# Optimization experiments

Hardware: AMD Instinct MI355X
Metric: run time of the kernel (lower is better)

## Reference

```python
import jax, jax.numpy as jnp
import numpy as np

HIDDEN = 512
NUM_HEADS = 8
HEAD_DIM = HIDDEN // NUM_HEADS


def setup_inputs() -> dict:
    key = jax.random.key(0)
    k1, k2 = jax.random.split(key)
    x = jax.random.normal(k1, (2, 2048, HIDDEN), dtype=jnp.float32)
    # torch Linear(h, 3h, bias=False): weight shape [3h, h], y = x @ W.T
    W_qkv = jax.random.normal(k2, (3 * HIDDEN, HIDDEN), dtype=jnp.float32) * (HIDDEN ** -0.5)
    return {"x": x, "W_qkv": W_qkv}


def reference(x, W_qkv):
    B, S, h = x.shape
    H, d = NUM_HEADS, HEAD_DIM
    temperature = (1.0 / d) ** 0.5  # sqrt(1/head_dim)
    qkv = x @ W_qkv.T  # [B, S, 3h]
    # Original chunks 3h into H pieces of size 3d (per-head interleaved QKV),
    # stacks on dim=1 -> [B, H, S, 3d], then splits into Q, K, V.
    qkv = qkv.reshape(B, S, H, 3 * d).transpose(0, 2, 1, 3)  # [B, H, S, 3d]
    q, k, v = jnp.split(qkv, 3, axis=-1)  # each [B, H, S, d]
    scores = jnp.einsum("bhqd,bhkd->bhqk", q * temperature, k)  # [B, H, S, S]
    # dropout is inference no-op; mask branch in original is a dead assignment
    w = jax.nn.softmax(scores, axis=-1)
    out = jnp.einsum("bhqk,bhkd->bhqd", w, v)  # [B, H, S, d]
    # torch.cat over heads on last dim == transpose back + merge heads
    return out.transpose(0, 2, 1, 3).reshape(B, S, h)
```

## Files before the change

kernel.cpp:

```cpp
#include <hip/hip_runtime.h>
#include <stdint.h>

#define HD 512
#define NH 8
#define DH 64
#define SEQ 2048
#define BATCH 2
#define M_TOTAL (BATCH*SEQ)
#define N_QKV (3*HD)
#define K_DIM HD

typedef short bf16x8 __attribute__((ext_vector_type(8)));
typedef float f32x4 __attribute__((ext_vector_type(4)));
typedef uint32_t u32x2 __attribute__((ext_vector_type(2)));
typedef uint32_t u32x4 __attribute__((ext_vector_type(4)));

#define QSCALE 0.18033688011112042f

__device__ __forceinline__ uint16_t f2bf(float f) {
  union { float f; uint32_t u; } v; v.f = f;
  uint32_t u = v.u;
  return (uint16_t)((u + 0x7FFFu + ((u >> 16) & 1u)) >> 16);
}

__device__ __forceinline__ void gload_lds16(const void* g, void* l) {
  __builtin_amdgcn_global_load_lds(
      (const __attribute__((address_space(1))) void*)g,
      (__attribute__((address_space(3))) void*)l,
      16, 0, 0);
}

__global__ void convert_f32_to_bf16(const float* __restrict__ in,
                                    uint16_t* __restrict__ out, int n4) {
  int i = blockIdx.x * blockDim.x + threadIdx.x;
  if (i < n4) {
    float4 v = reinterpret_cast<const float4*>(in)[i];
    ushort4 o;
    o.x = f2bf(v.x); o.y = f2bf(v.y); o.z = f2bf(v.z); o.w = f2bf(v.w);
    reinterpret_cast<ushort4*>(out)[i] = o;
  }
}

#define BM 128
#define BN 128
#define BK 64
#define NKT (K_DIM / BK)

__global__ __launch_bounds__(256)
void qkv_gemm(const uint16_t* __restrict__ A,
              const uint16_t* __restrict__ Bw,
              uint16_t* __restrict__ C,
              uint16_t* __restrict__ Vt) {
  __shared__ __align__(16) uint16_t As[2][BM * BK];
  __shared__ __align__(16) uint16_t Bs[2][BM * BK];

  const int t = threadIdx.x;
  const int lane = t & 63;
  const int w = t >> 6;
  const int wr = w >> 1, wc = w & 1;
  const int l15 = lane & 15, l4 = lane >> 4;

  const int nbx = gridDim.x;
  const int nwg = nbx * gridDim.y;
  const int cpx = nwg >> 3;
  int id = blockIdx.y * nbx + blockIdx.x;
  int wid = (id & 7) * cpx + (id >> 3);
  const int m0 = (wid / nbx) * BM;
  const int n0 = (wid % nbx) * BN;

  f32x4 acc[4][4] = {};

  auto stage = [&](int kt, int buf) {
#pragma unroll
    for (int i = 0; i < 4; ++i) {
      int idx = t + 256 * i;
      int row = idx >> 3, slot = idx & 7;
      int src = slot ^ (row & 7);
      gload_lds16(A + (size_t)(m0 + row) * K_DIM + kt * BK + src * 8,
                  (char*)As[buf] + idx * 16);
      gload_lds16(Bw + (size_t)(n0 + row) * K_DIM + kt * BK + src * 8,
                  (char*)Bs[buf] + idx * 16);
    }
  };

  stage(0, 0);
  for (int kt = 0; kt < NKT; ++kt) {
    __syncthreads();
    if (kt + 1 < NKT) stage(kt + 1, (kt + 1) & 1);
    const char* Ab = (const char*)As[kt & 1];
    const char* Bb = (const char*)Bs[kt & 1];
#pragma unroll
    for (int kk = 0; kk < 2; ++kk) {
      bf16x8 af[4], bfr[4];
#pragma unroll
      for (int i = 0; i < 4; ++i) {
        int rowa = wr * 64 + i * 16 + l15;
        int sa = (kk * 4 + l4) ^ (rowa & 7);
        af[i] = *reinterpret_cast<const bf16x8*>(Ab + rowa * 128 + sa * 16);
        int rowb = wc * 64 + i * 16 + l15;
        int sb = (kk * 4 + l4) ^ (rowb & 7);
        bfr[i] = *reinterpret_cast<const bf16x8*>(Bb + rowb * 128 + sb * 16);
      }
#pragma unroll
      for (int i = 0; i < 4; ++i)
#pragma unroll
        for (int j = 0; j < 4; ++j)
          acc[i][j] = __builtin_amdgcn_mfma_f32_16x16x32_bf16(af[i], bfr[j], acc[i][j], 0, 0, 0);
    }
  }

  const int colw = n0 + wc * 64;
  const bool isv = ((colw % 192) == 128);
  __syncthreads();

  if (isv) {
    char* tb = (char*)As + w * 8192;
#pragma unroll
    for (int i = 0; i < 4; ++i)
#pragma unroll
      for (int j = 0; j < 4; ++j) {
        uint32_t lo, hi;
        asm("v_cvt_pk_bf16_f32 %0, %1, %2" : "=v"(lo) : "v"(acc[i][j][0]), "v"(acc[i][j][1]));
        asm("v_cvt_pk_bf16_f32 %0, %1, %2" : "=v"(hi) : "v"(acc[i][j][2]), "v"(acc[i][j][3]));
        int dl = j * 16 + l15;
        int byteoff = dl * 128 + (((i * 2 + (l4 >> 1)) ^ (dl & 7)) * 16) + (l4 & 1) * 8;
        u32x2 pk; pk.x = lo; pk.y = hi;
        *reinterpret_cast<u32x2*>(tb + byteoff) = pk;
      }
    int h = colw / 192;
    int b = (m0 + wr * 64) >> 11;
    int sbase = (m0 + wr * 64) & (SEQ - 1);
    uint16_t* vbase = Vt + (size_t)(b * NH + h) * DH * SEQ + sbase + (lane & 7) * 8;
#pragma unroll
    for (int p = 0; p < 8; ++p) {
      int dl = p * 8 + (lane >> 3);
      u32x4 rv = *reinterpret_cast<const u32x4*>(
          tb + dl * 128 + (((lane & 7) ^ (dl & 7)) * 16));
      *reinterpret_cast<u32x4*>(vbase + (size_t)dl * SEQ) = rv;
    }
  } else {
#pragma unroll
    for (int i = 0; i < 4; ++i) {
      int row = m0 + wr * 64 + i * 16 + l4 * 4;
#pragma unroll
      for (int j = 0; j < 4; ++j) {
        int colb = colw + j * 16;
        int col = colb + l15;
        float sc = (((colb % 192) >> 6) == 0) ? QSCALE : 1.0f;
#pragma unroll
        for (int jj = 0; jj < 4; ++jj)
          C[(size_t)(row + jj) * N_QKV + col] = f2bf(acc[i][j][jj] * sc);
      }
    }
  }
}

#define NT (SEQ / 64)

__global__ __launch_bounds__(256)
void attn(const uint16_t* __restrict__ qkv, const uint16_t* __restrict__ VtG,
          float* __restrict__ Po,
          float2* __restrict__ Pml) {
  __shared__ __align__(16) uint16_t Kt[2][64 * 64];
  __shared__ __align__(16) uint16_t Vt[2][64 * 64];
  __shared__ __align__(16) uint16_t Pl[4][16 * 64];

  const int t = threadIdx.x;
  const int lane = t & 63;
  const int w = t >> 6;
  const int l15 = lane & 15, l4 = lane >> 4;
  const int bh = blockIdx.x;
  const int b = bh >> 3, h = bh & 7;
  const int q0 = blockIdx.y * 64;
  const int qw = q0 + w * 16;
  const int half = blockIdx.z;
  const int tph = NT / gridDim.z;
  const int t0 = half * tph;

  bf16x8 qf[2];
  {
    const uint16_t* qp = qkv + (size_t)(b * SEQ + qw + l15) * N_QKV + h * 192;
#pragma unroll
    for (int kk = 0; kk < 2; ++kk)
      qf[kk] = *reinterpret_cast<const bf16x8*>(qp + kk * 32 + l4 * 8);
  }

  const uint16_t* kgbase = qkv + (size_t)b * SEQ * N_QKV + h * 192 + 64;
  const uint16_t* vgbase = VtG + (size_t)bh * DH * SEQ;

  auto stage = [&](int ti, int buf) {
    int s0 = ti * 64;
#pragma unroll
    for (int i = 0; i < 2; ++i) {
      int idx = t + 256 * i;
      int row = idx >> 3, slot = idx & 7;
      int src = slot ^ (row & 7);
      gload_lds16(kgbase + (size_t)(s0 + row) * N_QKV + src * 8,
                  (char*)Kt[buf] + idx * 16);
      gload_lds16(vgbase + (size_t)row * SEQ + s0 + src * 8,
                  (char*)Vt[buf] + idx * 16);
    }
  };

  f32x4 o[4] = {};
  float mrow = -1e30f, lrow = 0.0f;

  stage(t0, 0);
  for (int rel = 0; rel < tph; ++rel) {
    int ti = t0 + rel;
    __syncthreads();
    if (rel + 1 < tph) stage(ti + 1, (rel + 1) & 1);
    const char* Kb = (const char*)Kt[rel & 1];
    const char* Vb = (const char*)Vt[rel & 1];

    f32x4 s[4] = {};
    __builtin_amdgcn_s_setprio(1);
#pragma unroll
    for (int c = 0; c < 4; ++c) {
#pragma unroll
      for (int kk = 0; kk < 2; ++kk) {
        int row = c * 16 + l15;
        int sl = (kk * 4 + l4) ^ (row & 7);
        bf16x8 kf = *reinterpret_cast<const bf16x8*>(Kb + row * 128 + sl * 16);
        s[c] = __builtin_amdgcn_mfma_f32_16x16x32_bf16(kf, qf[kk], s[c], 0, 0, 0);
      }
    }
    __builtin_amdgcn_s_setprio(0);

    float vmax = s[0][0];
#pragma unroll
    for (int c = 0; c < 4; ++c)
#pragma unroll
      for (int jj = 0; jj < 4; ++jj) vmax = fmaxf(vmax, s[c][jj]);
    vmax = fmaxf(vmax, __shfl_xor(vmax, 16, 64));
    vmax = fmaxf(vmax, __shfl_xor(vmax, 32, 64));

    if (!__all(vmax - mrow <= 11.0f)) {
      float mn = fmaxf(mrow, vmax);
      float sc;
      float darg = mrow - mn;
      asm("v_exp_f32 %0, %1" : "=v"(sc) : "v"(darg));
      mrow = mn;
      float sr[4];
#pragma unroll
      for (int jj = 0; jj < 4; ++jj) sr[jj] = __shfl(sc, l4 * 4 + jj, 64);
#pragma unroll
      for (int f = 0; f < 4; ++f)
#pragma unroll
        for (int jj = 0; jj < 4; ++jj) o[f][jj] *= sr[jj];
      lrow *= sc;
    }

    float p[16];
#pragma unroll
    for (int c = 0; c < 4; ++c)
#pragma unroll
      for (int jj = 0; jj < 4; ++jj) {
        float arg = s[c][jj] - mrow;
        float e;
        asm("v_exp_f32 %0, %1" : "=v"(e) : "v"(arg));
        p[c * 4 + jj] = e;
      }
    float a0 = (p[0] + p[1]) + (p[2] + p[3]);
    float a1 = (p[4] + p[5]) + (p[6] + p[7]);
    float a2 = (p[8] + p[9]) + (p[10] + p[11]);
    float a3 = (p[12] + p[13]) + (p[14] + p[15]);
    float tsum = (a0 + a1) + (a2 + a3);
    tsum += __shfl_xor(tsum, 16, 64);
    tsum += __shfl_xor(tsum, 32, 64);
    lrow += tsum;

#pragma unroll
    for (int c = 0; c < 4; ++c) {
      uint32_t lo, hi;
      asm("v_cvt_pk_bf16_f32 %0, %1, %2" : "=v"(lo) : "v"(p[c * 4 + 0]), "v"(p[c * 4 + 1]));
      asm("v_cvt_pk_bf16_f32 %0, %1, %2" : "=v"(hi) : "v"(p[c * 4 + 2]), "v"(p[c * 4 + 3]));
      int slot = 2 * c + (l4 >> 1);
      int byteoff = l15 * 128 + ((slot ^ (l15 & 7)) * 16) + (l4 & 1) * 8;
      u32x2 pk; pk.x = lo; pk.y = hi;
      *reinterpret_cast<u32x2*>((char*)Pl[w] + byteoff) = pk;
    }

    __builtin_amdgcn_s_setprio(1);
#pragma unroll
    for (int kk = 0; kk < 2; ++kk) {
      int sp = (kk * 4 + l4) ^ (l15 & 7);
      bf16x8 pa = *reinterpret_cast<const bf16x8*>((const char*)Pl[w] + l15 * 128 + sp * 16);
#pragma unroll
      for (int f = 0; f < 4; ++f) {
        int d = f * 16 + l15;
        int sv = (kk * 4 + l4) ^ (d & 7);
        bf16x8 vf = *reinterpret_cast<const bf16x8*>(Vb + d * 128 + sv * 16);
        o[f] = __builtin_amdgcn_mfma_f32_16x16x32_bf16(pa, vf, o[f], 0, 0, 0);
      }
    }
    __builtin_amdgcn_s_setprio(0);
  }

  float* pob = Po + ((size_t)(half * 16 + bh) * SEQ) * DH;
#pragma unroll
  for (int f = 0; f < 4; ++f) {
    int d = f * 16 + l15;
#pragma unroll
    for (int jj = 0; jj < 4; ++jj) {
      int q = qw + l4 * 4 + jj;
      pob[(size_t)q * DH + d] = o[f][jj];
    }
  }
  if (lane < 16) {
    float2 ml; ml.x = mrow; ml.y = lrow;
    Pml[(size_t)(half * 16 + bh) * SEQ + qw + lane] = ml;
  }
}

__global__ __launch_bounds__(256)
void attn_combine(const float* __restrict__ Po, const float2* __restrict__ Pml,
                  float* __restrict__ out, int nsplit) {
  int idx = blockIdx.x * 256 + threadIdx.x;
  int d4 = idx & 15;
  int q = (idx >> 4) & (SEQ - 1);
  int bh = idx >> 15;
  int b = bh >> 3, h = bh & 7;

  float2 ml0 = Pml[(size_t)bh * SEQ + q];
  f32x4 o0 = *reinterpret_cast<const f32x4*>(
      Po + ((size_t)bh * SEQ + q) * DH + d4 * 4);
  f32x4 res;
  if (nsplit == 2) {
    float2 ml1 = Pml[(size_t)(16 + bh) * SEQ + q];
    f32x4 o1 = *reinterpret_cast<const f32x4*>(
        Po + ((size_t)(16 + bh) * SEQ + q) * DH + d4 * 4);
    float m = fmaxf(ml0.x, ml1.x);
    float a0 = exp2f(ml0.x - m), a1 = exp2f(ml1.x - m);
    float rden = 1.0f / (ml0.y * a0 + ml1.y * a1);
#pragma unroll
    for (int i = 0; i < 4; ++i) res[i] = (o0[i] * a0 + o1[i] * a1) * rden;
  } else {
    float rden = 1.0f / ml0.y;
#pragma unroll
    for (int i = 0; i < 4; ++i) res[i] = o0[i] * rden;
  }
  *reinterpret_cast<f32x4*>(out + ((size_t)(b * SEQ + q) * HD) + h * 64 + d4 * 4) = res;
}

extern "C" void kernel_launch(void* const* d_in, const int* in_sizes, int n_in,
                              void* d_out, int out_size, void* d_ws, size_t ws_size,
                              hipStream_t stream) {
  const float* x = (const float*)d_in[0];
  const float* Wq = (const float*)d_in[1];
  float* out = (float*)d_out;

  uint16_t* xb = (uint16_t*)d_ws;
  uint16_t* Wb = xb + (size_t)M_TOTAL * K_DIM;
  uint16_t* qkv = Wb + (size_t)N_QKV * K_DIM;
  uint16_t* vtg = qkv + (size_t)M_TOTAL * N_QKV;
  float* Po = (float*)(vtg + (size_t)16 * DH * SEQ);
  float2* Pml = (float2*)(Po + (size_t)2 * 16 * SEQ * DH);
  size_t need2 = (char*)(Pml + (size_t)2 * 16 * SEQ) - (char*)d_ws;
  int nsplit = (ws_size >= need2) ? 2 : 1;

  convert_f32_to_bf16<<<(M_TOTAL * K_DIM / 4 + 255) / 256, 256, 0, stream>>>(
      x, xb, M_TOTAL * K_DIM / 4);
  convert_f32_to_bf16<<<(N_QKV * K_DIM / 4 + 255) / 256, 256, 0, stream>>>(
      Wq, Wb, N_QKV * K_DIM / 4);

  dim3 g1(N_QKV / BN, M_TOTAL / BM);
  qkv_gemm<<<g1, 256, 0, stream>>>(xb, Wb, qkv, vtg);

  dim3 g2(BATCH * NH, SEQ / 64, nsplit);
  attn<<<g2, 256, 0, stream>>>(qkv, vtg, Po, Pml);

  attn_combine<<<(16 * SEQ * 16) / 256, 256, 0, stream>>>(Po, Pml, out, nsplit);
}
```

Baseline: 114.6 us.

## Merge conversion kernels, shrink GEMM tile, register-staged attention with 4-way KV split

The two fp32→bf16 conversion launches become one kernel. The QKV GEMM M-tile shrinks from 128 to 64, with each wave owning a 64x32 output slice, which doubles the workgroup count. The attention kernel drops LDS double buffering and prefetches K/V through registers into a single LDS buffer, and adds an occupancy launch bound. The KV dimension is split four ways when the workspace allows, with a generalized combine kernel. The aim is more parallelism and occupancy. The cost is an extra barrier per tile, more combine traffic, and a Pml offset that assumes four splits even when only two fit.

```diff
diff --git a/kernel.cpp b/kernel.cpp
--- a/kernel.cpp
+++ b/kernel.cpp
@@ -30,18 +30,21 @@
       16, 0, 0);
 }
 
-__global__ void convert_f32_to_bf16(const float* __restrict__ in,
-                                    uint16_t* __restrict__ out, int n4) {
-  int i = blockIdx.x * blockDim.x + threadIdx.x;
-  if (i < n4) {
-    float4 v = reinterpret_cast<const float4*>(in)[i];
-    ushort4 o;
-    o.x = f2bf(v.x); o.y = f2bf(v.y); o.z = f2bf(v.z); o.w = f2bf(v.w);
-    reinterpret_cast<ushort4*>(out)[i] = o;
-  }
-}
-
-#define BM 128
+__global__ void convert_all(const float* __restrict__ x, const float* __restrict__ W,
+                            uint16_t* __restrict__ xb, uint16_t* __restrict__ Wb) {
+  const int nx4 = M_TOTAL * K_DIM / 4;
+  const int nw4 = N_QKV * K_DIM / 4;
+  int i = blockIdx.x * 256 + threadIdx.x;
+  const float* src; uint16_t* dst; int j;
+  if (i < nx4) { src = x; dst = xb; j = i; }
+  else { j = i - nx4; if (j >= nw4) return; src = W; dst = Wb; }
+  float4 v = reinterpret_cast<const float4*>(src)[j];
+  ushort4 o;
+  o.x = f2bf(v.x); o.y = f2bf(v.y); o.z = f2bf(v.z); o.w = f2bf(v.w);
+  reinterpret_cast<ushort4*>(dst)[j] = o;
+}
+
+#define BM 64
 #define BN 128
 #define BK 64
 #define NKT (K_DIM / BK)
@@ -52,12 +55,11 @@
               uint16_t* __restrict__ C,
               uint16_t* __restrict__ Vt) {
   __shared__ __align__(16) uint16_t As[2][BM * BK];
-  __shared__ __align__(16) uint16_t Bs[2][BM * BK];
+  __shared__ __align__(16) uint16_t Bs[2][BN * BK];
 
   const int t = threadIdx.x;
   const int lane = t & 63;
   const int w = t >> 6;
-  const int wr = w >> 1, wc = w & 1;
   const int l15 = lane & 15, l4 = lane >> 4;
 
   const int nbx = gridDim.x;
@@ -68,16 +70,22 @@
   const int m0 = (wid / nbx) * BM;
   const int n0 = (wid % nbx) * BN;
 
-  f32x4 acc[4][4] = {};
+  f32x4 acc[4][2] = {};
 
   auto stage = [&](int kt, int buf) {
 #pragma unroll
-    for (int i = 0; i < 4; ++i) {
+    for (int i = 0; i < 2; ++i) {
       int idx = t + 256 * i;
       int row = idx >> 3, slot = idx & 7;
       int src = slot ^ (row & 7);
       gload_lds16(A + (size_t)(m0 + row) * K_DIM + kt * BK + src * 8,
                   (char*)As[buf] + idx * 16);
+    }
+#pragma unroll
+    for (int i = 0; i < 4; ++i) {
+      int idx = t + 256 * i;
+      int row = idx >> 3, slot = idx & 7;
+      int src = slot ^ (row & 7);
       gload_lds16(Bw + (size_t)(n0 + row) * K_DIM + kt * BK + src * 8,
                   (char*)Bs[buf] + idx * 16);
     }
@@ -91,62 +99,67 @@
     const char* Bb = (const char*)Bs[kt & 1];
 #pragma unroll
     for (int kk = 0; kk < 2; ++kk) {
-      bf16x8 af[4], bfr[4];
+      bf16x8 af[4], bf[2];
 #pragma unroll
       for (int i = 0; i < 4; ++i) {
-        int rowa = wr * 64 + i * 16 + l15;
+        int rowa = i * 16 + l15;
         int sa = (kk * 4 + l4) ^ (rowa & 7);
         af[i] = *reinterpret_cast<const bf16x8*>(Ab + rowa * 128 + sa * 16);
-        int rowb = wc * 64 + i * 16 + l15;
+      }
+#pragma unroll
+      for (int j = 0; j < 2; ++j) {
+        int rowb = w * 32 + j * 16 + l15;
         int sb = (kk * 4 + l4) ^ (rowb & 7);
-        bfr[i] = *reinterpret_cast<const bf16x8*>(Bb + rowb * 128 + sb * 16);
+        bf[j] = *reinterpret_cast<const bf16x8*>(Bb + rowb * 128 + sb * 16);
       }
 #pragma unroll
       for (int i = 0; i < 4; ++i)
 #pragma unroll
-        for (int j = 0; j < 4; ++j)
-          acc[i][j] = __builtin_amdgcn_mfma_f32_16x16x32_bf16(af[i], bfr[j], acc[i][j], 0, 0, 0);
-    }
-  }
-
-  const int colw = n0 + wc * 64;
-  const bool isv = ((colw % 192) == 128);
+        for (int j = 0; j < 2; ++j)
+          acc[i][j] = __builtin_amdgcn_mfma_f32_16x16x32_bf16(af[i], bf[j], acc[i][j], 0, 0, 0);
+    }
+  }
+
+  const int colw = n0 + w * 32;
+  const int cmod = colw % 192;
+  const bool isv = (cmod >= 128);
   __syncthreads();
 
   if (isv) {
-    char* tb = (char*)As + w * 8192;
+    char* tb = (char*)As + w * 4096;
 #pragma unroll
     for (int i = 0; i < 4; ++i)
 #pragma unroll
-      for (int j = 0; j < 4; ++j) {
+      for (int j = 0; j < 2; ++j) {
         uint32_t lo, hi;
         asm("v_cvt_pk_bf16_f32 %0, %1, %2" : "=v"(lo) : "v"(acc[i][j][0]), "v"(acc[i][j][1]));
         asm("v_cvt_pk_bf16_f32 %0, %1, %2" : "=v"(hi) : "v"(acc[i][j][2]), "v"(acc[i][j][3]));
-        int dl = j * 16 + l15;
-        int byteoff = dl * 128 + (((i * 2 + (l4 >> 1)) ^ (dl & 7)) * 16) + (l4 & 1) * 8;
+        int dloc = j * 16 + l15;
+        int slot_s = i * 2 + (l4 >> 1);
+        int byteoff = dloc * 128 + ((slot_s ^ (dloc & 7)) * 16) + (l4 & 1) * 8;
         u32x2 pk; pk.x = lo; pk.y = hi;
         *reinterpret_cast<u32x2*>(tb + byteoff) = pk;
       }
     int h = colw / 192;
-    int b = (m0 + wr * 64) >> 11;
-    int sbase = (m0 + wr * 64) & (SEQ - 1);
-    uint16_t* vbase = Vt + (size_t)(b * NH + h) * DH * SEQ + sbase + (lane & 7) * 8;
-#pragma unroll
-    for (int p = 0; p < 8; ++p) {
+    int d0 = cmod - 128;
+    int b = m0 >> 11;
+    int sbase = m0 & (SEQ - 1);
+    uint16_t* vbase = Vt + ((size_t)(b * NH + h) * DH + d0) * SEQ + sbase + (lane & 7) * 8;
+#pragma unroll
+    for (int p = 0; p < 4; ++p) {
       int dl = p * 8 + (lane >> 3);
       u32x4 rv = *reinterpret_cast<const u32x4*>(
           tb + dl * 128 + (((lane & 7) ^ (dl & 7)) * 16));
       *reinterpret_cast<u32x4*>(vbase + (size_t)dl * SEQ) = rv;
     }
   } else {
+    float sc = ((cmod >> 6) == 0) ? QSCALE : 1.0f;
 #pragma unroll
     for (int i = 0; i < 4; ++i) {
-      int row = m0 + wr * 64 + i * 16 + l4 * 4;
-#pragma unroll
-      for (int j = 0; j < 4; ++j) {
-        int colb = colw + j * 16;
-        int col = colb + l15;
-        float sc = (((colb % 192) >> 6) == 0) ? QSCALE : 1.0f;
+      int row = m0 + i * 16 + l4 * 4;
+#pragma unroll
+      for (int j = 0; j < 2; ++j) {
+        int col = colw + j * 16 + l15;
 #pragma unroll
         for (int jj = 0; jj < 4; ++jj)
           C[(size_t)(row + jj) * N_QKV + col] = f2bf(acc[i][j][jj] * sc);
@@ -157,12 +170,12 @@
 
 #define NT (SEQ / 64)
 
-__global__ __launch_bounds__(256)
+__global__ __launch_bounds__(256, 6)
 void attn(const uint16_t* __restrict__ qkv, const uint16_t* __restrict__ VtG,
           float* __restrict__ Po,
           float2* __restrict__ Pml) {
-  __shared__ __align__(16) uint16_t Kt[2][64 * 64];
-  __shared__ __align__(16) uint16_t Vt[2][64 * 64];
+  __shared__ __align__(16) uint16_t Kt[64 * 64];
+  __shared__ __align__(16) uint16_t Vt[64 * 64];
   __shared__ __align__(16) uint16_t Pl[4][16 * 64];
 
   const int t = threadIdx.x;
@@ -171,8 +184,7 @@
   const int l15 = lane & 15, l4 = lane >> 4;
   const int bh = blockIdx.x;
   const int b = bh >> 3, h = bh & 7;
-  const int q0 = blockIdx.y * 64;
-  const int qw = q0 + w * 16;
+  const int qw = blockIdx.y * 64 + w * 16;
   const int half = blockIdx.z;
   const int tph = NT / gridDim.z;
   const int t0 = half * tph;
@@ -188,30 +200,41 @@
   const uint16_t* kgbase = qkv + (size_t)b * SEQ * N_QKV + h * 192 + 64;
   const uint16_t* vgbase = VtG + (size_t)bh * DH * SEQ;
 
-  auto stage = [&](int ti, int buf) {
+  u32x4 kreg[2], vreg[2];
+  auto loadrv = [&](int ti) {
     int s0 = ti * 64;
 #pragma unroll
     for (int i = 0; i < 2; ++i) {
       int idx = t + 256 * i;
       int row = idx >> 3, slot = idx & 7;
-      int src = slot ^ (row & 7);
-      gload_lds16(kgbase + (size_t)(s0 + row) * N_QKV + src * 8,
-                  (char*)Kt[buf] + idx * 16);
-      gload_lds16(vgbase + (size_t)row * SEQ + s0 + src * 8,
-                  (char*)Vt[buf] + idx * 16);
+      kreg[i] = *reinterpret_cast<const u32x4*>(
+          kgbase + (size_t)(s0 + row) * N_QKV + slot * 8);
+      vreg[i] = *reinterpret_cast<const u32x4*>(
+          vgbase + (size_t)row * SEQ + s0 + slot * 8);
+    }
+  };
+  auto writelds = [&]() {
+#pragma unroll
+    for (int i = 0; i < 2; ++i) {
+      int idx = t + 256 * i;
+      int row = idx >> 3, slot = idx & 7;
+      int off = row * 128 + ((slot ^ (row & 7)) * 16);
+      *reinterpret_cast<u32x4*>((char*)Kt + off) = kreg[i];
+      *reinterpret_cast<u32x4*>((char*)Vt + off) = vreg[i];
     }
   };
 
   f32x4 o[4] = {};
   float mrow = -1e30f, lrow = 0.0f;
 
-  stage(t0, 0);
+  loadrv(t0);
+  const char* Kb = (const char*)Kt;
+  const char* Vb = (const char*)Vt;
   for (int rel = 0; rel < tph; ++rel) {
-    int ti = t0 + rel;
     __syncthreads();
-    if (rel + 1 < tph) stage(ti + 1, (rel + 1) & 1);
-    const char* Kb = (const char*)Kt[rel & 1];
-    const char* Vb = (const char*)Vt[rel & 1];
+    writelds();
+    __syncthreads();
+    if (rel + 1 < tph) loadrv(t0 + rel + 1);
 
     f32x4 s[4] = {};
     __builtin_amdgcn_s_setprio(1);
@@ -322,24 +345,24 @@
   int bh = idx >> 15;
   int b = bh >> 3, h = bh & 7;
 
-  float2 ml0 = Pml[(size_t)bh * SEQ + q];
-  f32x4 o0 = *reinterpret_cast<const f32x4*>(
-      Po + ((size_t)bh * SEQ + q) * DH + d4 * 4);
+  float m = -1e30f;
+  for (int s = 0; s < nsplit; ++s)
+    m = fmaxf(m, Pml[(size_t)(s * 16 + bh) * SEQ + q].x);
+  float den = 0.0f;
+  f32x4 acc = {};
+  for (int s = 0; s < nsplit; ++s) {
+    float2 ml = Pml[(size_t)(s * 16 + bh) * SEQ + q];
+    float a = exp2f(ml.x - m);
+    den += ml.y * a;
+    f32x4 ov = *reinterpret_cast<const f32x4*>(
+        Po + ((size_t)(s * 16 + bh) * SEQ + q) * DH + d4 * 4);
+#pragma unroll
+    for (int i = 0; i < 4; ++i) acc[i] += ov[i] * a;
+  }
+  float rden = 1.0f / den;
   f32x4 res;
-  if (nsplit == 2) {
-    float2 ml1 = Pml[(size_t)(16 + bh) * SEQ + q];
-    f32x4 o1 = *reinterpret_cast<const f32x4*>(
-        Po + ((size_t)(16 + bh) * SEQ + q) * DH + d4 * 4);
-    float m = fmaxf(ml0.x, ml1.x);
-    float a0 = exp2f(ml0.x - m), a1 = exp2f(ml1.x - m);
-    float rden = 1.0f / (ml0.y * a0 + ml1.y * a1);
-#pragma unroll
-    for (int i = 0; i < 4; ++i) res[i] = (o0[i] * a0 + o1[i] * a1) * rden;
-  } else {
-    float rden = 1.0f / ml0.y;
-#pragma unroll
-    for (int i = 0; i < 4; ++i) res[i] = o0[i] * rden;
-  }
+#pragma unroll
+  for (int i = 0; i < 4; ++i) res[i] = acc[i] * rden;
   *reinterpret_cast<f32x4*>(out + ((size_t)(b * SEQ + q) * HD) + h * 64 + d4 * 4) = res;
 }
 
@@ -355,14 +378,15 @@
   uint16_t* qkv = Wb + (size_t)N_QKV * K_DIM;
   uint16_t* vtg = qkv + (size_t)M_TOTAL * N_QKV;
   float* Po = (float*)(vtg + (size_t)16 * DH * SEQ);
-  float2* Pml = (float2*)(Po + (size_t)2 * 16 * SEQ * DH);
-  size_t need2 = (char*)(Pml + (size_t)2 * 16 * SEQ) - (char*)d_ws;
-  int nsplit = (ws_size >= need2) ? 2 : 1;
-
-  convert_f32_to_bf16<<<(M_TOTAL * K_DIM / 4 + 255) / 256, 256, 0, stream>>>(
-      x, xb, M_TOTAL * K_DIM / 4);
-  convert_f32_to_bf16<<<(N_QKV * K_DIM / 4 + 255) / 256, 256, 0, stream>>>(
-      Wq, Wb, N_QKV * K_DIM / 4);
+  float2* Pml = (float2*)(Po + (size_t)4 * 16 * SEQ * DH);
+  size_t base = (size_t)((char*)Po - (char*)d_ws);
+  size_t per_split = (size_t)16 * SEQ * DH * 4 + (size_t)16 * SEQ * 8;
+  int nsplit = 1;
+  if (ws_size >= base + 4 * per_split) nsplit = 4;
+  else if (ws_size >= base + 2 * per_split) nsplit = 2;
+
+  convert_all<<<(M_TOTAL * K_DIM / 4 + N_QKV * K_DIM / 4 + 255) / 256, 256, 0, stream>>>(
+      x, Wq, xb, Wb);
 
   dim3 g1(N_QKV / BN, M_TOTAL / BM);
   qkv_gemm<<<g1, 256, 0, stream>>>(xb, Wb, qkv, vtg);
```

New measurement: 128.1 us. 1.12x slower.
